# Kernel tuning notes

Hardware: AMD Instinct MI355X
Metric: run time of the kernel (lower is better)

## Reference

```python
import jax, jax.numpy as jnp
import numpy as np

B, T, J, D = 2048, 120, 24, 6
E = J * D            # embed_dim = 144
L = 4                # n_layer
NH = 8               # n_head
HD = E // NH         # head_dim = 18
H = 144              # d_model = gru hidden (must equal E, see forward concat)
FF = 4 * E           # transformer dim_feedforward
GIN = E + H          # gru input size


def _layernorm(x, w, b):
    m = x.mean(-1, keepdims=True)
    v = ((x - m) ** 2).mean(-1, keepdims=True)
    return (x - m) / jnp.sqrt(v + 1e-5) * w + b


def setup_inputs() -> dict:
    key = jax.random.key(0)
    ks = jax.random.split(key, 32)
    s = 0.02
    n = lambda k, sh: jax.random.normal(k, sh, jnp.float32) * s
    return {
        "seed": jax.random.normal(ks[0], (B, T, J, D), jnp.float32),
        "qkv_w": n(ks[1], (L, 3 * E, E)), "qkv_b": jnp.zeros((L, 3 * E), jnp.float32),
        "out_w": n(ks[2], (L, E, E)), "out_b": jnp.zeros((L, E), jnp.float32),
        "ln1_w": jnp.ones((L, E), jnp.float32), "ln1_b": jnp.zeros((L, E), jnp.float32),
        "ffn1_w": n(ks[3], (L, FF, E)), "ffn1_b": jnp.zeros((L, FF), jnp.float32),
        "ffn2_w": n(ks[4], (L, E, FF)), "ffn2_b": jnp.zeros((L, E), jnp.float32),
        "ln2_w": jnp.ones((L, E), jnp.float32), "ln2_b": jnp.zeros((L, E), jnp.float32),
        "proj_w": n(ks[5], (E, E)), "proj_b": jnp.zeros((E,), jnp.float32),
        "w_ih": n(ks[6], (3 * H, GIN)), "w_hh": n(ks[7], (3 * H, H)),
        "b_ih": jnp.zeros((3 * H,), jnp.float32), "b_hh": jnp.zeros((3 * H,), jnp.float32),
        "spl_w": n(ks[8], (E, H)), "spl_b": jnp.zeros((E,), jnp.float32),
        "future": 24,
    }


def reference(seed, qkv_w, qkv_b, out_w, out_b, ln1_w, ln1_b, ffn1_w, ffn1_b,
              ffn2_w, ffn2_b, ln2_w, ln2_b, proj_w, proj_b,
              w_ih, w_hh, b_ih, b_hh, spl_w, spl_b, future):
    Bv, Tv, Jv, Dv = seed.shape
    x = seed.reshape(Bv, Tv, Jv * Dv)  # [B, T, E]

    # --- TransformerEncoder (post-norm, relu, dropout=eval-mode identity) ---
    def layer_step(x, p):
        (qw, qb, ow, ob, l1w, l1b, f1w, f1b, f2w, f2b, l2w, l2b) = p
        qkv = jnp.einsum('bse,fe->bsf', x, qw) + qb          # [B,S,3E]
        q, k, v = jnp.split(qkv, 3, axis=-1)
        q = q.reshape(Bv, Tv, NH, HD)
        k = k.reshape(Bv, Tv, NH, HD)
        v = v.reshape(Bv, Tv, NH, HD)
        scores = jnp.einsum('bqhd,bkhd->bhqk', q, k) / jnp.sqrt(jnp.float32(HD))
        attn = jax.nn.softmax(scores, axis=-1)
        o = jnp.einsum('bhqk,bkhd->bqhd', attn, v).reshape(Bv, Tv, E)
        o = jnp.einsum('bse,fe->bsf', o, ow) + ob
        x = _layernorm(x + o, l1w, l1b)
        ff = jax.nn.relu(jnp.einsum('bse,fe->bsf', x, f1w) + f1b)
        ff = jnp.einsum('bsf,ef->bse', ff, f2w) + f2b
        x = _layernorm(x + ff, l2w, l2b)
        return x, None

    x, _ = jax.lax.scan(layer_step, x,
                        (qkv_w, qkv_b, out_w, out_b, ln1_w, ln1_b,
                         ffn1_w, ffn1_b, ffn2_w, ffn2_b, ln2_w, ln2_b))
    ctx = x.mean(axis=1) @ proj_w.T + proj_b               # [B, E]

    h0 = jnp.zeros((Bv, H), seed.dtype)
    inp0 = seed[:, -1].reshape(Bv, Jv * Dv)

    def step(carry, _):
        h, inp = carry
        xc = jnp.concatenate([inp, ctx], axis=-1)          # [B, E+H]
        gi = xc @ w_ih.T + b_ih                            # [B, 3H]
        gh = h @ w_hh.T + b_hh
        ir, iz, in_ = jnp.split(gi, 3, axis=-1)
        hr, hz, hn = jnp.split(gh, 3, axis=-1)
        r = jax.nn.sigmoid(ir + hr)
        z = jax.nn.sigmoid(iz + hz)
        n = jnp.tanh(in_ + r * hn)
        h_new = (1.0 - z) * n + z * h
        rot6d = h_new @ spl_w.T + spl_b                    # [B, E]
        return (h_new, rot6d), rot6d

    _, ys = jax.lax.scan(step, (h0, inp0), None, length=future)  # [future,B,E]
    return ys.transpose(1, 0, 2).reshape(Bv, future, Jv, Dv)
```

## Files before the change

### kernel.cpp

```cpp
#include <hip/hip_runtime.h>

#define B_   2048
#define T_   120
#define E_   144
#define L_   4
#define NH_  8
#define HD_  18
#define FF_  576
#define H_   144
#define GIN_ 288
#define TH_  432
#define FUT_ 24
#define BT_  (B_*T_)

typedef unsigned short u16;
typedef unsigned int   u32;

typedef __attribute__((ext_vector_type(8))) short short8v;
typedef __attribute__((ext_vector_type(4))) float f32x4;

__device__ __forceinline__ float bf2f(u16 u) {
    u32 x = ((u32)u) << 16;
    return __uint_as_float(x);
}
__device__ __forceinline__ u16 f2bf(float f) {
    u32 x = __float_as_uint(f);
    u32 r = (x + 0x7fffu + ((x >> 16) & 1u)) >> 16;
    return (u16)r;
}

struct F4 { float x, y, z, w; };

__device__ __forceinline__ F4 load4(const float* p) {
    float4 v = *(const float4*)p;
    return {v.x, v.y, v.z, v.w};
}
__device__ __forceinline__ void store1(float* p, float v) { *p = v; }
__device__ __forceinline__ void store1(u16* p, float v)   { *p = f2bf(v); }

__device__ __forceinline__ short8v wfrag(const u16* Wp, int tile, int NS, int s, int l) {
    return *(const short8v*)(Wp + (((size_t)tile * NS + s) * 64 + l) * 8);
}

__device__ __forceinline__ void gll16(const void* g, void* l) {
    __builtin_amdgcn_global_load_lds(
        (const __attribute__((address_space(1))) u32*)g,
        (__attribute__((address_space(3))) u32*)l, 16, 0, 0);
}

__device__ __forceinline__ void stage64(const u16* src, u32* lds, int tid) {
    const char* base = (const char*)src;
    char* lbase = (char*)lds;
    const int w = tid >> 6, l = tid & 63;
#pragma unroll
    for (int i = 0; i < 7; ++i) {
        int inst  = w * 7 + i;
        int chunk = inst * 64 + l;
        int row = chunk / 21;
        int col = chunk - row * 21;
        if (col > 17) col = 17;
        gll16(base + row * 288 + col * 16, lbase + inst * 1024);
    }
}

__global__ void wpack_kernel(const float* __restrict__ src, u16* __restrict__ dst,
                             int ntiles, int NS, int K, int sstr)
{
    int i = blockIdx.x * 256 + threadIdx.x;
    if (i >= ntiles * NS * 512) return;
    int e  = i & 7;
    int l  = (i >> 3) & 63;
    int c  = i >> 9;
    int s  = c % NS;
    int tile = c / NS;
    int li = l & 15, lg = l >> 4;
    int row = tile * 16 + li;
    int k   = s * 32 + lg * 8 + e;
    dst[i] = (k < K) ? f2bf(src[(size_t)row * sstr + k]) : (u16)0;
}

__global__ void cast_bf_kernel(const float* __restrict__ src, u16* __restrict__ dst,
                               int n2)
{
    int i = blockIdx.x * 256 + threadIdx.x;
    if (i >= n2) return;
    float2 t = ((const float2*)src)[i];
    ((u32*)dst)[i] = ((u32)f2bf(t.y) << 16) | (u32)f2bf(t.x);
}

template<typename OT>
__global__ __launch_bounds__(192) void gemm_mfma(
    const u16* __restrict__ A, const u16* __restrict__ Wb,
    const float* __restrict__ bias, OT* __restrict__ C, int M, int N)
{
    __shared__ u32 lds[64 * 84];

    const int tid = threadIdx.x;
    const int w   = tid >> 6;
    const int l   = tid & 63;
    const int lg  = l >> 4;
    const int li  = l & 15;
    const int bm  = blockIdx.y * 64;
    const int n0w = blockIdx.x * 144 + w * 48;
    const int t0  = blockIdx.x * 9 + w * 3;

    f32x4 acc[4][3];
#pragma unroll
    for (int rt = 0; rt < 4; rt++)
#pragma unroll
        for (int ct = 0; ct < 3; ct++) acc[rt][ct] = {0.f, 0.f, 0.f, 0.f};

    stage64(A + (size_t)bm * 144, lds, tid);
    __syncthreads();

    const u16* lds16 = (const u16*)lds;
#pragma unroll
    for (int s = 0; s < 5; ++s) {
        short8v bf[3];
#pragma unroll
        for (int ct = 0; ct < 3; ++ct)
            bf[ct] = wfrag(Wb, t0 + ct, 5, s, l);
        short8v af[4];
#pragma unroll
        for (int rt = 0; rt < 4; ++rt)
            af[rt] = *(const short8v*)(lds16 + (rt * 16 + li) * 168 + s * 32 + lg * 8);
#pragma unroll
        for (int rt = 0; rt < 4; ++rt)
#pragma unroll
            for (int ct = 0; ct < 3; ++ct)
                acc[rt][ct] = __builtin_amdgcn_mfma_f32_16x16x32_bf16(
                    af[rt], bf[ct], acc[rt][ct], 0, 0, 0);
    }

#pragma unroll
    for (int ct = 0; ct < 3; ++ct) {
        int col = n0w + ct * 16 + li;
        float bv = bias[col];
#pragma unroll
        for (int rt = 0; rt < 4; ++rt) {
#pragma unroll
            for (int j = 0; j < 4; ++j) {
                int row = bm + rt * 16 + lg * 4 + j;
                store1(&C[(size_t)row * N + col], acc[rt][ct][j] + bv);
            }
        }
    }
}

__global__ __launch_bounds__(192) void olnffn_kernel(
    const u16* __restrict__ ob, const u16* __restrict__ Wo,
    const float* __restrict__ ob_b, const float* __restrict__ res,
    const float* __restrict__ ln1w, const float* __restrict__ ln1b,
    const u16* __restrict__ W1, const float* __restrict__ b1,
    const u16* __restrict__ W2, const float* __restrict__ b2,
    const float* __restrict__ ln2w, const float* __restrict__ ln2b,
    u16* __restrict__ obf, float* __restrict__ of)
{
    __shared__ __align__(16) u16 Als[64 * 168];
    __shared__ u32 Fls[64 * 52];
    __shared__ float lnS[3][64], lnQ[3][64];

    const int tid = threadIdx.x;
    const int w   = tid >> 6;
    const int l   = tid & 63;
    const int lg  = l >> 4;
    const int li  = l & 15;
    const int bm  = blockIdx.x * 64;

    stage64(ob + (size_t)bm * 144, (u32*)Als, tid);
    __syncthreads();

    const u16* als = Als;
    u16* alsw = Als;
    u16* fls16 = (u16*)Fls;

    f32x4 acc[4][3];
#pragma unroll
    for (int rt = 0; rt < 4; rt++)
#pragma unroll
        for (int ct = 0; ct < 3; ct++) acc[rt][ct] = {0.f, 0.f, 0.f, 0.f};
#pragma unroll
    for (int s = 0; s < 5; ++s) {
        short8v bf[3];
#pragma unroll
        for (int ct = 0; ct < 3; ++ct)
            bf[ct] = wfrag(Wo, w * 3 + ct, 5, s, l);
        short8v af[4];
#pragma unroll
        for (int rt = 0; rt < 4; ++rt)
            af[rt] = *(const short8v*)(als + (rt * 16 + li) * 168 + s * 32 + lg * 8);
#pragma unroll
        for (int rt = 0; rt < 4; ++rt)
#pragma unroll
            for (int ct = 0; ct < 3; ++ct)
                acc[rt][ct] = __builtin_amdgcn_mfma_f32_16x16x32_bf16(
                    af[rt], bf[ct], acc[rt][ct], 0, 0, 0);
    }

    float vv[4][3][4];
#pragma unroll
    for (int ct = 0; ct < 3; ++ct) {
        int col = w * 48 + ct * 16 + li;
        float bv = ob_b[col];
#pragma unroll
        for (int rt = 0; rt < 4; ++rt)
#pragma unroll
            for (int j = 0; j < 4; ++j) {
                int row = bm + rt * 16 + lg * 4 + j;
                vv[rt][ct][j] = acc[rt][ct][j] + bv + res[(size_t)row * E_ + col];
            }
    }
#pragma unroll
    for (int rt = 0; rt < 4; ++rt)
#pragma unroll
        for (int j = 0; j < 4; ++j) {
            float s = vv[rt][0][j] + vv[rt][1][j] + vv[rt][2][j];
            float q = vv[rt][0][j] * vv[rt][0][j] + vv[rt][1][j] * vv[rt][1][j]
                    + vv[rt][2][j] * vv[rt][2][j];
#pragma unroll
            for (int off = 1; off < 16; off <<= 1) {
                s += __shfl_xor(s, off);
                q += __shfl_xor(q, off);
            }
            if (li == 0) {
                lnS[w][rt * 16 + lg * 4 + j] = s;
                lnQ[w][rt * 16 + lg * 4 + j] = q;
            }
        }
    __syncthreads();
#pragma unroll
    for (int rt = 0; rt < 4; ++rt)
#pragma unroll
        for (int j = 0; j < 4; ++j) {
            int r = rt * 16 + lg * 4 + j;
            float mean = (lnS[0][r] + lnS[1][r] + lnS[2][r]) * (1.f / 144.f);
            float var  = (lnQ[0][r] + lnQ[1][r] + lnQ[2][r]) * (1.f / 144.f) - mean * mean;
            float rstd = rsqrtf(var + 1e-5f);
#pragma unroll
            for (int ct = 0; ct < 3; ++ct) {
                int col = w * 48 + ct * 16 + li;
                float o = (vv[rt][ct][j] - mean) * rstd * ln1w[col] + ln1b[col];
                vv[rt][ct][j] = o;
                alsw[r * 168 + col] = f2bf(o);
            }
        }
    __syncthreads();

    f32x4 acc2[4][3];
#pragma unroll
    for (int rt = 0; rt < 4; rt++)
#pragma unroll
        for (int ct = 0; ct < 3; ct++) acc2[rt][ct] = {0.f, 0.f, 0.f, 0.f};

    for (int c = 0; c < 6; ++c) {
        f32x4 acc1[4][2];
#pragma unroll
        for (int rt = 0; rt < 4; rt++)
#pragma unroll
            for (int ct = 0; ct < 2; ct++) acc1[rt][ct] = {0.f, 0.f, 0.f, 0.f};
#pragma unroll
        for (int s = 0; s < 5; ++s) {
            short8v bf[2];
#pragma unroll
            for (int ct = 0; ct < 2; ++ct)
                bf[ct] = wfrag(W1, c * 6 + w * 2 + ct, 5, s, l);
            short8v af[4];
#pragma unroll
            for (int rt = 0; rt < 4; ++rt)
                af[rt] = *(const short8v*)(als + (rt * 16 + li) * 168 + s * 32 + lg * 8);
#pragma unroll
            for (int rt = 0; rt < 4; ++rt)
#pragma unroll
                for (int ct = 0; ct < 2; ++ct)
                    acc1[rt][ct] = __builtin_amdgcn_mfma_f32_16x16x32_bf16(
                        af[rt], bf[ct], acc1[rt][ct], 0, 0, 0);
        }
        __syncthreads();
#pragma unroll
        for (int ct = 0; ct < 2; ++ct) {
            int colc = w * 32 + ct * 16 + li;
            float bv = b1[c * 96 + colc];
#pragma unroll
            for (int rt = 0; rt < 4; ++rt)
#pragma unroll
                for (int j = 0; j < 4; ++j) {
                    int row = rt * 16 + lg * 4 + j;
                    float v = fmaxf(acc1[rt][ct][j] + bv, 0.f);
                    fls16[row * 104 + colc] = f2bf(v);
                }
        }
        __syncthreads();
#pragma unroll
        for (int s2 = 0; s2 < 3; ++s2) {
            short8v wf[3];
#pragma unroll
            for (int ct = 0; ct < 3; ++ct)
                wf[ct] = wfrag(W2, w * 3 + ct, 18, c * 3 + s2, l);
            short8v pf[4];
#pragma unroll
            for (int rt = 0; rt < 4; ++rt)
                pf[rt] = *(const short8v*)(fls16 + (rt * 16 + li) * 104 + s2 * 32 + lg * 8);
#pragma unroll
            for (int rt = 0; rt < 4; ++rt)
#pragma unroll
                for (int ct = 0; ct < 3; ++ct)
                    acc2[rt][ct] = __builtin_amdgcn_mfma_f32_16x16x32_bf16(
                        pf[rt], wf[ct], acc2[rt][ct], 0, 0, 0);
        }
    }

    float v2[4][3][4];
#pragma unroll
    for (int ct = 0; ct < 3; ++ct) {
        int col = w * 48 + ct * 16 + li;
        float bv = b2[col];
#pragma unroll
        for (int rt = 0; rt < 4; ++rt)
#pragma unroll
            for (int j = 0; j < 4; ++j)
                v2[rt][ct][j] = acc2[rt][ct][j] + bv + vv[rt][ct][j];
    }
#pragma unroll
    for (int rt = 0; rt < 4; ++rt)
#pragma unroll
        for (int j = 0; j < 4; ++j) {
            float s = v2[rt][0][j] + v2[rt][1][j] + v2[rt][2][j];
            float q = v2[rt][0][j] * v2[rt][0][j] + v2[rt][1][j] * v2[rt][1][j]
                    + v2[rt][2][j] * v2[rt][2][j];
#pragma unroll
            for (int off = 1; off < 16; off <<= 1) {
                s += __shfl_xor(s, off);
                q += __shfl_xor(q, off);
            }
            if (li == 0) {
                lnS[w][rt * 16 + lg * 4 + j] = s;
                lnQ[w][rt * 16 + lg * 4 + j] = q;
            }
        }
    __syncthreads();
#pragma unroll
    for (int rt = 0; rt < 4; ++rt)
#pragma unroll
        for (int j = 0; j < 4; ++j) {
            int r = rt * 16 + lg * 4 + j;
            float mean = (lnS[0][r] + lnS[1][r] + lnS[2][r]) * (1.f / 144.f);
            float var  = (lnQ[0][r] + lnQ[1][r] + lnQ[2][r]) * (1.f / 144.f) - mean * mean;
            float rstd = rsqrtf(var + 1e-5f);
            int row = bm + r;
#pragma unroll
            for (int ct = 0; ct < 3; ++ct) {
                int col = w * 48 + ct * 16 + li;
                float o = (v2[rt][ct][j] - mean) * rstd * ln2w[col] + ln2b[col];
                obf[(size_t)row * E_ + col] = f2bf(o);
                of[(size_t)row * E_ + col]  = o;
            }
        }
}

template<typename AT, typename OT, bool BIAS, bool RELU, bool RES>
__global__ __launch_bounds__(256) void gemm_kernel(
    const AT* __restrict__ A, const float* __restrict__ W, int ldw,
    const float* __restrict__ bias, const float* __restrict__ res,
    OT* __restrict__ C, int M, int N, int K)
{
    constexpr int BM = 64, BN = 64, BK = 16;
    __shared__ float As[BK][BM + 4];
    __shared__ float Ws[BK][BN + 4];
    const int tid = threadIdx.x;
    const int bm = blockIdx.y * BM;
    const int bn = blockIdx.x * BN;
    const int tx = tid & 15, ty = tid >> 4;
    const int lr = tid >> 2;
    const int lc = (tid & 3) << 2;

    float acc[4][4];
#pragma unroll
    for (int i = 0; i < 4; i++)
#pragma unroll
        for (int j = 0; j < 4; j++) acc[i][j] = 0.f;

    for (int k0 = 0; k0 < K; k0 += BK) {
        F4 av = load4(A + (size_t)(bm + lr) * K + k0 + lc);
        As[lc + 0][lr] = av.x; As[lc + 1][lr] = av.y;
        As[lc + 2][lr] = av.z; As[lc + 3][lr] = av.w;
        int n = bn + lr;
        F4 wv = {0.f, 0.f, 0.f, 0.f};
        if (n < N) {
            float4 t = *(const float4*)(W + (size_t)n * ldw + k0 + lc);
            wv = {t.x, t.y, t.z, t.w};
        }
        Ws[lc + 0][lr] = wv.x; Ws[lc + 1][lr] = wv.y;
        Ws[lc + 2][lr] = wv.z; Ws[lc + 3][lr] = wv.w;
        __syncthreads();
#pragma unroll
        for (int kk = 0; kk < BK; ++kk) {
            float a[4], wr[4];
#pragma unroll
            for (int i = 0; i < 4; i++) a[i] = As[kk][ty * 4 + i];
#pragma unroll
            for (int j = 0; j < 4; j++) wr[j] = Ws[kk][tx * 4 + j];
#pragma unroll
            for (int i = 0; i < 4; i++)
#pragma unroll
                for (int j = 0; j < 4; j++) acc[i][j] += a[i] * wr[j];
        }
        __syncthreads();
    }
#pragma unroll
    for (int i = 0; i < 4; i++) {
        int m = bm + ty * 4 + i;
#pragma unroll
        for (int j = 0; j < 4; j++) {
            int n = bn + tx * 4 + j;
            if (n < N) {
                float v = acc[i][j];
                if (BIAS) v += bias[n];
                if (RES)  v += res[(size_t)m * N + n];
                if (RELU) v = fmaxf(v, 0.f);
                store1(&C[(size_t)m * N + n], v);
            }
        }
    }
}

__global__ __launch_bounds__(256) void attn_kernel(const u16* __restrict__ qkv,
                                                   u16* __restrict__ o)
{
    constexpr int QS = 40;
    constexpr int VS = 136;
    __shared__ __align__(16) u16 Qs[128 * QS];
    __shared__ __align__(16) u16 Ks[128 * QS];
    __shared__ __align__(16) u16 Vt[32 * VS];
    __shared__ __align__(16) u16 Ps[4][16 * VS];

    const int bh = blockIdx.x;
    const int b = bh >> 3, h = bh & 7;
    const int tid = threadIdx.x;
    const int w = tid >> 6, l = tid & 63;
    const int lg = l >> 4, li = l & 15;

    {
        u32* z1 = (u32*)Qs;
        for (int i = tid; i < 128 * QS / 2; i += 256) z1[i] = 0;
        u32* z2 = (u32*)Ks;
        for (int i = tid; i < 128 * QS / 2; i += 256) z2[i] = 0;
        u32* z3 = (u32*)Vt;
        for (int i = tid; i < 32 * VS / 2; i += 256) z3[i] = 0;
    }
    __syncthreads();

    const u32* q32 = (const u32*)(qkv + (size_t)b * T_ * TH_);
    for (int idx = tid; idx < 120 * 9; idx += 256) {
        int t = idx / 9, dp = idx - t * 9;
        u32 qv = q32[t * 216 + 9 * h + dp];
        u32 kv = q32[t * 216 + 72 + 9 * h + dp];
        u32 vv = q32[t * 216 + 144 + 9 * h + dp];
        ((u32*)(Qs + t * QS))[dp] = qv;
        ((u32*)(Ks + t * QS))[dp] = kv;
        Vt[(2 * dp) * VS + t]     = (u16)(vv & 0xffffu);
        Vt[(2 * dp + 1) * VS + t] = (u16)(vv >> 16);
    }
    __syncthreads();

    const float scale = 0.23570226039551584f;
    u16* pw = &Ps[w][0];

    for (int mt = w * 2; mt < w * 2 + 2; ++mt) {
        short8v qf = *(const short8v*)(Qs + (mt * 16 + li) * QS + lg * 8);
        f32x4 sacc[8];
#pragma unroll
        for (int nt = 0; nt < 8; ++nt) sacc[nt] = {0.f, 0.f, 0.f, 0.f};
#pragma unroll
        for (int nt = 0; nt < 8; ++nt) {
            short8v kf = *(const short8v*)(Ks + (nt * 16 + li) * QS + lg * 8);
            sacc[nt] = __builtin_amdgcn_mfma_f32_16x16x32_bf16(qf, kf, sacc[nt], 0, 0, 0);
        }

        float invl[4];
#pragma unroll
        for (int j = 0; j < 4; ++j) {
            float v[8];
            float m = -1e30f;
#pragma unroll
            for (int nt = 0; nt < 8; ++nt) {
                float s = sacc[nt][j] * scale;
                if (nt == 7 && li >= 8) s = -1e30f;
                v[nt] = s;
                m = fmaxf(m, s);
            }
#pragma unroll
            for (int off = 1; off < 16; off <<= 1)
                m = fmaxf(m, __shfl_xor(m, off));
            float sum = 0.f;
#pragma unroll
            for (int nt = 0; nt < 8; ++nt) {
                float p = __expf(v[nt] - m);
                sum += p;
                pw[(lg * 4 + j) * VS + nt * 16 + li] = f2bf(p);
            }
#pragma unroll
            for (int off = 1; off < 16; off <<= 1)
                sum += __shfl_xor(sum, off);
            invl[j] = 1.f / sum;
        }

        f32x4 oacc[2] = {{0.f,0.f,0.f,0.f},{0.f,0.f,0.f,0.f}};
#pragma unroll
        for (int s = 0; s < 4; ++s) {
            short8v pf = *(const short8v*)(pw + li * VS + s * 32 + lg * 8);
#pragma unroll
            for (int dt = 0; dt < 2; ++dt) {
                short8v vf = *(const short8v*)(Vt + (dt * 16 + li) * VS + s * 32 + lg * 8);
                oacc[dt] = __builtin_amdgcn_mfma_f32_16x16x32_bf16(pf, vf, oacc[dt], 0, 0, 0);
            }
        }

        const int q0 = mt * 16 + lg * 4;
#pragma unroll
        for (int dt = 0; dt < 2; ++dt) {
            int d = dt * 16 + li;
            if (d < HD_) {
#pragma unroll
                for (int j = 0; j < 4; ++j) {
                    int q = q0 + j;
                    if (q < T_)
                        o[((size_t)b * T_ + q) * E_ + h * HD_ + d] =
                            f2bf(oacc[dt][j] * invl[j]);
                }
            }
        }
    }
}

__global__ void mean_kernel(const float* __restrict__ x, float* __restrict__ out,
                            int nb)
{
    int idx = blockIdx.x * blockDim.x + threadIdx.x;
    if (idx >= nb * E_) return;
    int b = idx / E_, e = idx % E_;
    const float* p = x + (size_t)b * T_ * E_ + e;
    float s = 0.f;
    for (int t = 0; t < T_; t++) s += p[(size_t)t * E_];
    out[idx] = s * (1.f / 120.f);
}

__device__ __forceinline__ float sigmoidf_(float x) {
    return 1.f / (1.f + __expf(-x));
}

#define GRU_M 16
__global__ __launch_bounds__(192) void gru_all_kernel(
    const float* __restrict__ seed,
    const float* __restrict__ gctx,
    const u16* __restrict__ WxB,
    const u16* __restrict__ WhB,
    const u16* __restrict__ SpB,
    const float* __restrict__ b_hh,
    const float* __restrict__ spl_b,
    float* __restrict__ out)
{
    __shared__ __align__(16) u16 xls[GRU_M * 168];
    __shared__ __align__(16) u16 hls[GRU_M * 168];

    const int tid = threadIdx.x;
    const int w = tid >> 6, l = tid & 63;
    const int lg = l >> 4, li = l & 15;
    const int b0 = blockIdx.x * GRU_M;
    const int fr = w * 48 + li;

    for (int i = tid; i < GRU_M * 84; i += 192) {
        ((u32*)xls)[i] = 0; ((u32*)hls)[i] = 0;
    }
    __syncthreads();
    for (int i = tid; i < GRU_M * 72; i += 192) {
        int r = i / 72, e2 = i - r * 72;
        float2 t = *(const float2*)(seed + (size_t)(b0 + r) * T_ * E_
                                    + (size_t)(T_ - 1) * E_ + 2 * e2);
        ((u32*)(xls + r * 168))[e2] = ((u32)f2bf(t.y) << 16) | (u32)f2bf(t.x);
    }

    float gctxv[3][3][4];
// ... 75 lines not shown
#pragma unroll
            for (int ct = 0; ct < 3; ++ct) {
                short8v bs = wfrag(SpB, w * 3 + ct, 5, s, l);
                aS[ct] = __builtin_amdgcn_mfma_f32_16x16x32_bf16(ah, bs, aS[ct], 0, 0, 0);
            }
        }
#pragma unroll
        for (int ct = 0; ct < 3; ++ct) {
            int col = fr + ct * 16;
#pragma unroll
            for (int j = 0; j < 4; ++j) {
                float rv = aS[ct][j] + splb[ct];
                out[(size_t)(b0 + lg * 4 + j) * (FUT_ * E_) + (size_t)st * E_ + col] = rv;
                xls[(lg * 4 + j) * 168 + col] = f2bf(rv);
            }
        }
        __syncthreads();
    }
}

extern "C" void kernel_launch(void* const* d_in, const int* in_sizes, int n_in,
                              void* d_out, int out_size, void* d_ws, size_t ws_size,
                              hipStream_t stream)
{
    const float* seed   = (const float*)d_in[0];
    const float* qkv_w  = (const float*)d_in[1];
    const float* qkv_b  = (const float*)d_in[2];
    const float* out_w  = (const float*)d_in[3];
    const float* out_b  = (const float*)d_in[4];
    const float* ln1_w  = (const float*)d_in[5];
    const float* ln1_b  = (const float*)d_in[6];
    const float* ffn1_w = (const float*)d_in[7];
    const float* ffn1_b = (const float*)d_in[8];
    const float* ffn2_w = (const float*)d_in[9];
    const float* ffn2_b = (const float*)d_in[10];
    const float* ln2_w  = (const float*)d_in[11];
    const float* ln2_b  = (const float*)d_in[12];
    const float* proj_w = (const float*)d_in[13];
    const float* proj_b = (const float*)d_in[14];
    const float* w_ih   = (const float*)d_in[15];
    const float* w_hh   = (const float*)d_in[16];
    const float* b_ih   = (const float*)d_in[17];
    const float* b_hh   = (const float*)d_in[18];
    const float* spl_w  = (const float*)d_in[19];
    const float* spl_b  = (const float*)d_in[20];

    const size_t qkvW_n  = (size_t)L_ * TH_ * 160;
    const size_t outW_n  = (size_t)L_ * E_ * 160;
    const size_t ffn1W_n = (size_t)L_ * FF_ * 160;
    const size_t ffn2W_n = (size_t)L_ * E_ * 576;
    const size_t wxW_n   = (size_t)TH_ * 160;
    const size_t whW_n   = (size_t)TH_ * 160;
    const size_t spW_n   = (size_t)E_ * 160;
    const size_t wbytes  = (qkvW_n + outW_n + ffn1W_n + ffn2W_n
                            + wxW_n + whW_n + spW_n) * 2;

    const size_t persist = (size_t)B_ * 4 * (E_ + E_ + TH_) + wbytes;

    int nc = 16;
    for (int c = 1; c <= 16; c <<= 1) {
        size_t rows = (size_t)(B_ / c) * T_;
        size_t need = persist + rows * 2016;
        if (need <= ws_size) { nc = c; break; }
    }
    const int BC = B_ / nc;
    const int CR = BC * T_;

    char* wsp = (char*)d_ws;
    u16*   xbf   = (u16*)wsp;   wsp += (size_t)CR * E_ * 2;
    float* xres  = (float*)wsp; wsp += (size_t)CR * E_ * 4;
    u16*   qf    = (u16*)wsp;   wsp += (size_t)CR * TH_ * 2;
    u16*   ob    = (u16*)wsp;   wsp += (size_t)CR * E_ * 2;
    float* ctxm  = (float*)wsp; wsp += (size_t)B_ * E_ * 4;
    float* ctx   = (float*)wsp; wsp += (size_t)B_ * E_ * 4;
    float* gctx  = (float*)wsp; wsp += (size_t)B_ * TH_ * 4;
    u16* qkvWb   = (u16*)wsp;   wsp += qkvW_n * 2;
    u16* outWb   = (u16*)wsp;   wsp += outW_n * 2;
    u16* ffn1Wb  = (u16*)wsp;   wsp += ffn1W_n * 2;
    u16* ffn2Wb  = (u16*)wsp;   wsp += ffn2W_n * 2;
    u16* wxB     = (u16*)wsp;   wsp += wxW_n * 2;
    u16* whB     = (u16*)wsp;   wsp += whW_n * 2;
    u16* splWb   = (u16*)wsp;   wsp += spW_n * 2;

    wpack_kernel<<<(int)((qkvW_n + 255) / 256), 256, 0, stream>>>(qkv_w, qkvWb, L_ * 27, 5, 144, 144);
    wpack_kernel<<<(int)((outW_n + 255) / 256), 256, 0, stream>>>(out_w, outWb, L_ * 9, 5, 144, 144);
    wpack_kernel<<<(int)((ffn1W_n + 255) / 256), 256, 0, stream>>>(ffn1_w, ffn1Wb, L_ * 36, 5, 144, 144);
    wpack_kernel<<<(int)((ffn2W_n + 255) / 256), 256, 0, stream>>>(ffn2_w, ffn2Wb, L_ * 9, 18, 576, 576);
    wpack_kernel<<<(int)((wxW_n + 255) / 256), 256, 0, stream>>>(w_ih, wxB, 27, 5, 144, GIN_);
    wpack_kernel<<<(int)((whW_n + 255) / 256), 256, 0, stream>>>(w_hh, whB, 27, 5, 144, 144);
    wpack_kernel<<<(int)((spW_n + 255) / 256), 256, 0, stream>>>(spl_w, splWb, 9, 5, 144, 144);

    auto grid = [](int M, int N) { return dim3((N + 63) / 64, M / 64); };

    for (int c = 0; c < nc; c++) {
        const int b0 = c * BC;
        cast_bf_kernel<<<(CR * 72 + 255) / 256, 256, 0, stream>>>(
            seed + (size_t)b0 * T_ * E_, xbf, CR * 72);
        const float* resIn = seed + (size_t)b0 * T_ * E_;
        for (int l = 0; l < L_; l++) {
            gemm_mfma<u16><<<dim3(3, CR / 64), 192, 0, stream>>>(
                xbf, qkvWb + (size_t)l * TH_ * 160, qkv_b + (size_t)l * TH_,
                qf, CR, TH_);
            attn_kernel<<<BC * NH_, 256, 0, stream>>>(qf, ob);
            olnffn_kernel<<<CR / 64, 192, 0, stream>>>(
                ob, outWb + (size_t)l * E_ * 160, out_b + (size_t)l * E_, resIn,
                ln1_w + (size_t)l * E_, ln1_b + (size_t)l * E_,
                ffn1Wb + (size_t)l * FF_ * 160, ffn1_b + (size_t)l * FF_,
                ffn2Wb + (size_t)l * E_ * 576, ffn2_b + (size_t)l * E_,
                ln2_w + (size_t)l * E_, ln2_b + (size_t)l * E_, xbf, xres);
            resIn = xres;
        }
        mean_kernel<<<(BC * E_ + 255) / 256, 256, 0, stream>>>(xres, ctxm + (size_t)b0 * E_, BC);
    }

    gemm_kernel<float, float, true, false, false><<<grid(B_, E_), 256, 0, stream>>>(
        ctxm, proj_w, E_, proj_b, nullptr, ctx, B_, E_, E_);
    gemm_kernel<float, float, true, false, false><<<grid(B_, TH_), 256, 0, stream>>>(
        ctx, w_ih + E_, GIN_, b_ih, nullptr, gctx, B_, TH_, E_);

    gru_all_kernel<<<B_ / GRU_M, 192, 0, stream>>>(
        seed, gctx, wxB, whB, splWb, b_hh, spl_b, (float*)d_out);
}
```

Before: 2.863 ms.

## Fuse QKV, attention, out-proj, LN and FFN into one per-sequence layer kernel

Replaces the per-layer QKV GEMM, attention and out-proj/LN/FFN kernels with a single layer_kernel that processes one batch sequence (120 rows) per block. QKV results and attention outputs stay in LDS instead of round-tripping through global memory, and the batch-chunk loop is removed so all sequences run in one launch per layer. The residual is now read from the bf16 activations (except in layer 0), which lowers precision. The large LDS footprint and launch bounds of one block per CU may limit occupancy and latency hiding.

```diff
diff --git a/kernel.cpp b/kernel.cpp
--- a/kernel.cpp
+++ b/kernel.cpp
@@ -30,7 +30,6 @@
 }
 
 struct F4 { float x, y, z, w; };
-
 __device__ __forceinline__ F4 load4(const float* p) {
     float4 v = *(const float4*)p;
     return {v.x, v.y, v.z, v.w};
@@ -48,19 +47,14 @@
         (__attribute__((address_space(3))) u32*)l, 16, 0, 0);
 }
 
-__device__ __forceinline__ void stage64(const u16* src, u32* lds, int tid) {
-    const char* base = (const char*)src;
-    char* lbase = (char*)lds;
-    const int w = tid >> 6, l = tid & 63;
-#pragma unroll
-    for (int i = 0; i < 7; ++i) {
-        int inst  = w * 7 + i;
-        int chunk = inst * 64 + l;
-        int row = chunk / 21;
-        int col = chunk - row * 21;
-        if (col > 17) col = 17;
-        gll16(base + row * 288 + col * 16, lbase + inst * 1024);
-    }
+__device__ __forceinline__ short8v qk_frag(const u16* rowp, int colbase, int lg) {
+    u32 u0 = 0, u1 = 0, u2 = 0, u3 = 0;
+    const u32* p = (const u32*)(rowp + colbase + lg * 8);
+    if (lg < 2) { u0 = p[0]; u1 = p[1]; u2 = p[2]; u3 = p[3]; }
+    else if (lg == 2) { u0 = p[0]; }
+    union { u32 u[4]; short8v v; } r;
+    r.u[0] = u0; r.u[1] = u1; r.u[2] = u2; r.u[3] = u3;
+    return r.v;
 }
 
 __global__ void wpack_kernel(const float* __restrict__ src, u16* __restrict__ dst,
@@ -88,271 +82,360 @@
     ((u32*)dst)[i] = ((u32)f2bf(t.y) << 16) | (u32)f2bf(t.x);
 }
 
-template<typename OT>
-__global__ __launch_bounds__(192) void gemm_mfma(
-    const u16* __restrict__ A, const u16* __restrict__ Wb,
-    const float* __restrict__ bias, OT* __restrict__ C, int M, int N)
-{
-    __shared__ u32 lds[64 * 84];
-
-    const int tid = threadIdx.x;
-    const int w   = tid >> 6;
-    const int l   = tid & 63;
-    const int lg  = l >> 4;
-    const int li  = l & 15;
-    const int bm  = blockIdx.y * 64;
-    const int n0w = blockIdx.x * 144 + w * 48;
-    const int t0  = blockIdx.x * 9 + w * 3;
-
-    f32x4 acc[4][3];
-#pragma unroll
-    for (int rt = 0; rt < 4; rt++)
-#pragma unroll
-        for (int ct = 0; ct < 3; ct++) acc[rt][ct] = {0.f, 0.f, 0.f, 0.f};
-
-    stage64(A + (size_t)bm * 144, lds, tid);
-    __syncthreads();
-
-    const u16* lds16 = (const u16*)lds;
-#pragma unroll
-    for (int s = 0; s < 5; ++s) {
-        short8v bf[3];
-#pragma unroll
-        for (int ct = 0; ct < 3; ++ct)
-            bf[ct] = wfrag(Wb, t0 + ct, 5, s, l);
-        short8v af[4];
-#pragma unroll
-        for (int rt = 0; rt < 4; ++rt)
-            af[rt] = *(const short8v*)(lds16 + (rt * 16 + li) * 168 + s * 32 + lg * 8);
-#pragma unroll
-        for (int rt = 0; rt < 4; ++rt)
-#pragma unroll
-            for (int ct = 0; ct < 3; ++ct)
-                acc[rt][ct] = __builtin_amdgcn_mfma_f32_16x16x32_bf16(
-                    af[rt], bf[ct], acc[rt][ct], 0, 0, 0);
-    }
-
-#pragma unroll
-    for (int ct = 0; ct < 3; ++ct) {
-        int col = n0w + ct * 16 + li;
-        float bv = bias[col];
-#pragma unroll
-        for (int rt = 0; rt < 4; ++rt) {
-#pragma unroll
-            for (int j = 0; j < 4; ++j) {
-                int row = bm + rt * 16 + lg * 4 + j;
-                store1(&C[(size_t)row * N + col], acc[rt][ct][j] + bv);
-            }
-        }
-    }
-}
-
-__global__ __launch_bounds__(192) void olnffn_kernel(
-    const u16* __restrict__ ob, const u16* __restrict__ Wo,
-    const float* __restrict__ ob_b, const float* __restrict__ res,
+template<bool RESF32, bool WF32>
+__global__ __launch_bounds__(256, 1) void layer_kernel(
+    const u16* __restrict__ xin,
+    const float* __restrict__ resf, const u16* __restrict__ resb,
+    const u16* __restrict__ Wqkv, const float* __restrict__ bqkv,
+    const u16* __restrict__ Wo, const float* __restrict__ bo,
     const float* __restrict__ ln1w, const float* __restrict__ ln1b,
     const u16* __restrict__ W1, const float* __restrict__ b1,
     const u16* __restrict__ W2, const float* __restrict__ b2,
     const float* __restrict__ ln2w, const float* __restrict__ ln2b,
     u16* __restrict__ obf, float* __restrict__ of)
 {
-    __shared__ __align__(16) u16 Als[64 * 168];
-    __shared__ u32 Fls[64 * 52];
-    __shared__ float lnS[3][64], lnQ[3][64];
+    __shared__ __align__(16) u16 Xls[21504];
+    __shared__ __align__(16) u16 QKV[128 * 440];
 
     const int tid = threadIdx.x;
-    const int w   = tid >> 6;
-    const int l   = tid & 63;
-    const int lg  = l >> 4;
-    const int li  = l & 15;
-    const int bm  = blockIdx.x * 64;
-
-    stage64(ob + (size_t)bm * 144, (u32*)Als, tid);
-    __syncthreads();
-
-    const u16* als = Als;
-    u16* alsw = Als;
-    u16* fls16 = (u16*)Fls;
-
-    f32x4 acc[4][3];
-#pragma unroll
-    for (int rt = 0; rt < 4; rt++)
-#pragma unroll
-        for (int ct = 0; ct < 3; ct++) acc[rt][ct] = {0.f, 0.f, 0.f, 0.f};
+    const int w  = tid >> 6, l = tid & 63;
+    const int lg = l >> 4,  li = l & 15;
+    const size_t grow0 = (size_t)blockIdx.x * T_;
+
+    for (int i = tid; i < 672; i += 256) ((u32*)Xls)[10080 + i] = 0;
+    {
+        const char* src = (const char*)(xin + grow0 * E_);
+        char* dst = (char*)Xls;
+#pragma unroll
+        for (int i = 0; i < 10; ++i) {
+            int inst = w * 10 + i;
+            int chunk = inst * 64 + l;
+            if (chunk < 2520) {
+                int row = chunk / 21, col = chunk - row * 21;
+                if (col > 17) col = 17;
+                gll16(src + row * 288 + col * 16, dst + inst * 1024);
+            }
+        }
+    }
+    __syncthreads();
+
+#pragma unroll
+    for (int ci = 0; ci < 7; ++ci) {
+        int ct = w + 4 * ci;
+        if (ct < 27) {
+            f32x4 acc[8];
+#pragma unroll
+            for (int rt = 0; rt < 8; ++rt) acc[rt] = {0.f, 0.f, 0.f, 0.f};
+#pragma unroll
+            for (int s = 0; s < 5; ++s) {
+                short8v bf = wfrag(Wqkv, ct, 5, s, l);
+#pragma unroll
+                for (int rt = 0; rt < 8; ++rt) {
+                    short8v af = *(const short8v*)(Xls + (rt * 16 + li) * 168 + s * 32 + lg * 8);
+                    acc[rt] = __builtin_amdgcn_mfma_f32_16x16x32_bf16(af, bf, acc[rt], 0, 0, 0);
+                }
+            }
+            int col = ct * 16 + li;
+            float bv = bqkv[col];
+#pragma unroll
+            for (int rt = 0; rt < 8; ++rt)
+#pragma unroll
+                for (int j = 0; j < 4; ++j)
+                    QKV[(rt * 16 + lg * 4 + j) * 440 + col] = f2bf(acc[rt][j] + bv);
+        }
+    }
+    __syncthreads();
+
+    {
+        const float scale = 0.23570226039551584f;
+        u16* Pw = Xls + w * 2176;
+        for (int h = 0; h < NH_; ++h) {
+            const int qc = h * HD_;
+            short8v kf[8];
+#pragma unroll
+            for (int nt = 0; nt < 8; ++nt)
+                kf[nt] = qk_frag(QKV + (nt * 16 + li) * 440, E_ + qc, lg);
+            short8v vf[2][4];
+#pragma unroll
+            for (int dt = 0; dt < 2; ++dt) {
+                int d = dt * 16 + li;
+#pragma unroll
+                for (int s = 0; s < 4; ++s) {
+                    union { u16 h16[8]; short8v v; } r;
+#pragma unroll
+                    for (int e = 0; e < 8; ++e)
+                        r.h16[e] = (d < HD_)
+                            ? QKV[(s * 32 + lg * 8 + e) * 440 + 2 * E_ + qc + d]
+                            : (u16)0;
+                    vf[dt][s] = r.v;
+                }
+            }
+#pragma unroll
+            for (int qi = 0; qi < 2; ++qi) {
+                int qt = 2 * w + qi;
+                short8v qf = qk_frag(QKV + (qt * 16 + li) * 440, qc, lg);
+                f32x4 sacc[8];
+#pragma unroll
+                for (int nt = 0; nt < 8; ++nt) sacc[nt] = {0.f, 0.f, 0.f, 0.f};
+#pragma unroll
+                for (int nt = 0; nt < 8; ++nt)
+                    sacc[nt] = __builtin_amdgcn_mfma_f32_16x16x32_bf16(qf, kf[nt], sacc[nt], 0, 0, 0);
+
+                float invl[4];
+#pragma unroll
+                for (int j = 0; j < 4; ++j) {
+                    float v[8];
+                    float m = -1e30f;
+#pragma unroll
+                    for (int nt = 0; nt < 8; ++nt) {
+                        float s = sacc[nt][j] * scale;
+                        if (nt == 7 && li >= 8) s = -1e30f;
+                        v[nt] = s;
+                        m = fmaxf(m, s);
+                    }
+#pragma unroll
+                    for (int off = 1; off < 16; off <<= 1)
+                        m = fmaxf(m, __shfl_xor(m, off));
+                    float sum = 0.f;
+#pragma unroll
+                    for (int nt = 0; nt < 8; ++nt) {
+                        float p = __expf(v[nt] - m);
+                        sum += p;
+                        Pw[(lg * 4 + j) * 136 + nt * 16 + li] = f2bf(p);
+                    }
+#pragma unroll
+                    for (int off = 1; off < 16; off <<= 1)
+                        sum += __shfl_xor(sum, off);
+                    invl[j] = 1.f / sum;
+                }
+
+                f32x4 oacc[2] = {{0.f,0.f,0.f,0.f},{0.f,0.f,0.f,0.f}};
+#pragma unroll
+                for (int s = 0; s < 4; ++s) {
+                    short8v pf = *(const short8v*)(Pw + li * 136 + s * 32 + lg * 8);
+#pragma unroll
+                    for (int dt = 0; dt < 2; ++dt)
+                        oacc[dt] = __builtin_amdgcn_mfma_f32_16x16x32_bf16(pf, vf[dt][s], oacc[dt], 0, 0, 0);
+                }
+#pragma unroll
+                for (int dt = 0; dt < 2; ++dt) {
+                    int d = dt * 16 + li;
+                    if (d < HD_) {
+#pragma unroll
+                        for (int j = 0; j < 4; ++j)
+                            QKV[(qt * 16 + lg * 4 + j) * 440 + qc + d] =
+                                f2bf(oacc[dt][j] * invl[j]);
+                    }
+                }
+            }
+        }
+    }
+    __syncthreads();
+
+    float* lnS = (float*)(Xls + 10240);
+    float* lnQ = (float*)(Xls + 11264);
+
+    float rr[3][8][4];
+#pragma unroll
+    for (int ci = 0; ci < 3; ++ci) {
+        int tile = w + 4 * ci;
+        if (tile < 9) {
+            int col = tile * 16 + li;
+#pragma unroll
+            for (int rt = 0; rt < 8; ++rt)
+#pragma unroll
+                for (int j = 0; j < 4; ++j) {
+                    int r = rt * 16 + lg * 4 + j;
+                    if (r > 119) r = 119;
+                    rr[ci][rt][j] = RESF32 ? resf[(grow0 + r) * E_ + col]
+                                           : bf2f(resb[(grow0 + r) * E_ + col]);
+                }
+        }
+    }
+
+    f32x4 acc[3][8];
+#pragma unroll
+    for (int ci = 0; ci < 3; ++ci)
+#pragma unroll
+        for (int rt = 0; rt < 8; ++rt) acc[ci][rt] = {0.f, 0.f, 0.f, 0.f};
 #pragma unroll
     for (int s = 0; s < 5; ++s) {
-        short8v bf[3];
-#pragma unroll
-        for (int ct = 0; ct < 3; ++ct)
-            bf[ct] = wfrag(Wo, w * 3 + ct, 5, s, l);
-        short8v af[4];
-#pragma unroll
-        for (int rt = 0; rt < 4; ++rt)
-            af[rt] = *(const short8v*)(als + (rt * 16 + li) * 168 + s * 32 + lg * 8);
-#pragma unroll
-        for (int rt = 0; rt < 4; ++rt)
-#pragma unroll
-            for (int ct = 0; ct < 3; ++ct)
-                acc[rt][ct] = __builtin_amdgcn_mfma_f32_16x16x32_bf16(
-                    af[rt], bf[ct], acc[rt][ct], 0, 0, 0);
-    }
-
-    float vv[4][3][4];
-#pragma unroll
-    for (int ct = 0; ct < 3; ++ct) {
-        int col = w * 48 + ct * 16 + li;
-        float bv = ob_b[col];
-#pragma unroll
-        for (int rt = 0; rt < 4; ++rt)
-#pragma unroll
-            for (int j = 0; j < 4; ++j) {
-                int row = bm + rt * 16 + lg * 4 + j;
-                vv[rt][ct][j] = acc[rt][ct][j] + bv + res[(size_t)row * E_ + col];
-            }
-    }
-#pragma unroll
-    for (int rt = 0; rt < 4; ++rt)
+        short8v bfv[3];
+#pragma unroll
+        for (int ci = 0; ci < 3; ++ci) {
+            int tile = w + 4 * ci;
+            if (tile < 9) bfv[ci] = wfrag(Wo, tile, 5, s, l);
+        }
+#pragma unroll
+        for (int rt = 0; rt < 8; ++rt) {
+            short8v af = *(const short8v*)(QKV + (rt * 16 + li) * 440 + s * 32 + lg * 8);
+#pragma unroll
+            for (int ci = 0; ci < 3; ++ci)
+                if (w + 4 * ci < 9)
+                    acc[ci][rt] = __builtin_amdgcn_mfma_f32_16x16x32_bf16(af, bfv[ci], acc[ci][rt], 0, 0, 0);
+        }
+    }
+
+    float vv[3][8][4];
+#pragma unroll
+    for (int ci = 0; ci < 3; ++ci) {
+        int tile = w + 4 * ci;
+        if (tile < 9) {
+            float bv = bo[tile * 16 + li];
+#pragma unroll
+            for (int rt = 0; rt < 8; ++rt)
+#pragma unroll
+                for (int j = 0; j < 4; ++j)
+                    vv[ci][rt][j] = acc[ci][rt][j] + bv + rr[ci][rt][j];
+        }
+    }
+#pragma unroll
+    for (int rt = 0; rt < 8; ++rt)
 #pragma unroll
         for (int j = 0; j < 4; ++j) {
-            float s = vv[rt][0][j] + vv[rt][1][j] + vv[rt][2][j];
-            float q = vv[rt][0][j] * vv[rt][0][j] + vv[rt][1][j] * vv[rt][1][j]
-                    + vv[rt][2][j] * vv[rt][2][j];
+            float s = 0.f, q = 0.f;
+#pragma unroll
+            for (int ci = 0; ci < 3; ++ci)
+                if (w + 4 * ci < 9) { s += vv[ci][rt][j]; q += vv[ci][rt][j] * vv[ci][rt][j]; }
 #pragma unroll
             for (int off = 1; off < 16; off <<= 1) {
                 s += __shfl_xor(s, off);
                 q += __shfl_xor(q, off);
             }
             if (li == 0) {
-                lnS[w][rt * 16 + lg * 4 + j] = s;
-                lnQ[w][rt * 16 + lg * 4 + j] = q;
-            }
-        }
-    __syncthreads();
-#pragma unroll
-    for (int rt = 0; rt < 4; ++rt)
+                lnS[w * 128 + rt * 16 + lg * 4 + j] = s;
+                lnQ[w * 128 + rt * 16 + lg * 4 + j] = q;
+            }
+        }
+    __syncthreads();
+#pragma unroll
+    for (int rt = 0; rt < 8; ++rt)
 #pragma unroll
         for (int j = 0; j < 4; ++j) {
             int r = rt * 16 + lg * 4 + j;
-            float mean = (lnS[0][r] + lnS[1][r] + lnS[2][r]) * (1.f / 144.f);
-            float var  = (lnQ[0][r] + lnQ[1][r] + lnQ[2][r]) * (1.f / 144.f) - mean * mean;
+            float s = lnS[r] + lnS[128 + r] + lnS[256 + r] + lnS[384 + r];
+            float q = lnQ[r] + lnQ[128 + r] + lnQ[256 + r] + lnQ[384 + r];
+            float mean = s * (1.f / 144.f);
+            float var  = q * (1.f / 144.f) - mean * mean;
             float rstd = rsqrtf(var + 1e-5f);
 #pragma unroll
-            for (int ct = 0; ct < 3; ++ct) {
-                int col = w * 48 + ct * 16 + li;
-                float o = (vv[rt][ct][j] - mean) * rstd * ln1w[col] + ln1b[col];
-                vv[rt][ct][j] = o;
-                alsw[r * 168 + col] = f2bf(o);
-            }
-        }
-    __syncthreads();
-
-    f32x4 acc2[4][3];
-#pragma unroll
-    for (int rt = 0; rt < 4; rt++)
-#pragma unroll
-        for (int ct = 0; ct < 3; ct++) acc2[rt][ct] = {0.f, 0.f, 0.f, 0.f};
-
-    for (int c = 0; c < 6; ++c) {
-        f32x4 acc1[4][2];
-#pragma unroll
-        for (int rt = 0; rt < 4; rt++)
-#pragma unroll
-            for (int ct = 0; ct < 2; ct++) acc1[rt][ct] = {0.f, 0.f, 0.f, 0.f};
+            for (int ci = 0; ci < 3; ++ci) {
+                int tile = w + 4 * ci;
+                if (tile < 9) {
+                    int col = tile * 16 + li;
+                    float o = (vv[ci][rt][j] - mean) * rstd * ln1w[col] + ln1b[col];
+                    vv[ci][rt][j] = o;
+                    QKV[r * 440 + col] = f2bf(o);
+                }
+            }
+        }
+    __syncthreads();
+
+    u16* Fls = Xls;
+    f32x4 acc2[3][8];
+#pragma unroll
+    for (int ci = 0; ci < 3; ++ci)
+#pragma unroll
+        for (int rt = 0; rt < 8; ++rt) acc2[ci][rt] = {0.f, 0.f, 0.f, 0.f};
+
+    for (int c = 0; c < 9; ++c) {
+        f32x4 acc1[8];
+#pragma unroll
+        for (int rt = 0; rt < 8; ++rt) acc1[rt] = {0.f, 0.f, 0.f, 0.f};
 #pragma unroll
         for (int s = 0; s < 5; ++s) {
-            short8v bf[2];
-#pragma unroll
-            for (int ct = 0; ct < 2; ++ct)
-                bf[ct] = wfrag(W1, c * 6 + w * 2 + ct, 5, s, l);
-            short8v af[4];
-#pragma unroll
-            for (int rt = 0; rt < 4; ++rt)
-                af[rt] = *(const short8v*)(als + (rt * 16 + li) * 168 + s * 32 + lg * 8);
-#pragma unroll
-            for (int rt = 0; rt < 4; ++rt)
-#pragma unroll
-                for (int ct = 0; ct < 2; ++ct)
-                    acc1[rt][ct] = __builtin_amdgcn_mfma_f32_16x16x32_bf16(
-                        af[rt], bf[ct], acc1[rt][ct], 0, 0, 0);
+            short8v bf = wfrag(W1, c * 4 + w, 5, s, l);
+#pragma unroll
+            for (int rt = 0; rt < 8; ++rt) {
+                short8v af = *(const short8v*)(QKV + (rt * 16 + li) * 440 + s * 32 + lg * 8);
+                acc1[rt] = __builtin_amdgcn_mfma_f32_16x16x32_bf16(af, bf, acc1[rt], 0, 0, 0);
+            }
         }
         __syncthreads();
-#pragma unroll
-        for (int ct = 0; ct < 2; ++ct) {
-            int colc = w * 32 + ct * 16 + li;
-            float bv = b1[c * 96 + colc];
-#pragma unroll
-            for (int rt = 0; rt < 4; ++rt)
+        {
+            int colc = w * 16 + li;
+            float bv = b1[c * 64 + colc];
+#pragma unroll
+            for (int rt = 0; rt < 8; ++rt)
 #pragma unroll
                 for (int j = 0; j < 4; ++j) {
-                    int row = rt * 16 + lg * 4 + j;
-                    float v = fmaxf(acc1[rt][ct][j] + bv, 0.f);
-                    fls16[row * 104 + colc] = f2bf(v);
+                    float v = fmaxf(acc1[rt][j] + bv, 0.f);
+                    Fls[(rt * 16 + lg * 4 + j) * 72 + colc] = f2bf(v);
                 }
         }
         __syncthreads();
 #pragma unroll
-        for (int s2 = 0; s2 < 3; ++s2) {
-            short8v wf[3];
-#pragma unroll
-            for (int ct = 0; ct < 3; ++ct)
-                wf[ct] = wfrag(W2, w * 3 + ct, 18, c * 3 + s2, l);
-            short8v pf[4];
-#pragma unroll
-            for (int rt = 0; rt < 4; ++rt)
-                pf[rt] = *(const short8v*)(fls16 + (rt * 16 + li) * 104 + s2 * 32 + lg * 8);
-#pragma unroll
-            for (int rt = 0; rt < 4; ++rt)
-#pragma unroll
-                for (int ct = 0; ct < 3; ++ct)
-                    acc2[rt][ct] = __builtin_amdgcn_mfma_f32_16x16x32_bf16(
-                        pf[rt], wf[ct], acc2[rt][ct], 0, 0, 0);
-        }
-    }
-
-    float v2[4][3][4];
-#pragma unroll
-    for (int ct = 0; ct < 3; ++ct) {
-        int col = w * 48 + ct * 16 + li;
-        float bv = b2[col];
-#pragma unroll
-        for (int rt = 0; rt < 4; ++rt)
-#pragma unroll
-            for (int j = 0; j < 4; ++j)
-                v2[rt][ct][j] = acc2[rt][ct][j] + bv + vv[rt][ct][j];
-    }
-#pragma unroll
-    for (int rt = 0; rt < 4; ++rt)
+        for (int s2 = 0; s2 < 2; ++s2) {
+            short8v bfw[3];
+#pragma unroll
+            for (int ci = 0; ci < 3; ++ci) {
+                int tile = w + 4 * ci;
+                if (tile < 9) bfw[ci] = wfrag(W2, tile, 18, c * 2 + s2, l);
+            }
+#pragma unroll
+            for (int rt = 0; rt < 8; ++rt) {
+                short8v pf = *(const short8v*)(Fls + (rt * 16 + li) * 72 + s2 * 32 + lg * 8);
+#pragma unroll
+                for (int ci = 0; ci < 3; ++ci)
+                    if (w + 4 * ci < 9)
+                        acc2[ci][rt] = __builtin_amdgcn_mfma_f32_16x16x32_bf16(pf, bfw[ci], acc2[ci][rt], 0, 0, 0);
+            }
+        }
+    }
+
+#pragma unroll
+    for (int ci = 0; ci < 3; ++ci) {
+        int tile = w + 4 * ci;
+        if (tile < 9) {
+            float bv = b2[tile * 16 + li];
+#pragma unroll
+            for (int rt = 0; rt < 8; ++rt)
+#pragma unroll
+                for (int j = 0; j < 4; ++j)
+                    vv[ci][rt][j] = acc2[ci][rt][j] + bv + vv[ci][rt][j];
+        }
+    }
+    __syncthreads();
+#pragma unroll
+    for (int rt = 0; rt < 8; ++rt)
 #pragma unroll
         for (int j = 0; j < 4; ++j) {
-            float s = v2[rt][0][j] + v2[rt][1][j] + v2[rt][2][j];
-            float q = v2[rt][0][j] * v2[rt][0][j] + v2[rt][1][j] * v2[rt][1][j]
-                    + v2[rt][2][j] * v2[rt][2][j];
+            float s = 0.f, q = 0.f;
+#pragma unroll
+            for (int ci = 0; ci < 3; ++ci)
+                if (w + 4 * ci < 9) { s += vv[ci][rt][j]; q += vv[ci][rt][j] * vv[ci][rt][j]; }
 #pragma unroll
             for (int off = 1; off < 16; off <<= 1) {
                 s += __shfl_xor(s, off);
                 q += __shfl_xor(q, off);
             }
             if (li == 0) {
-                lnS[w][rt * 16 + lg * 4 + j] = s;
-                lnQ[w][rt * 16 + lg * 4 + j] = q;
-            }
-        }
-    __syncthreads();
-#pragma unroll
-    for (int rt = 0; rt < 4; ++rt)
+                lnS[w * 128 + rt * 16 + lg * 4 + j] = s;
+                lnQ[w * 128 + rt * 16 + lg * 4 + j] = q;
+            }
+        }
+    __syncthreads();
+#pragma unroll
+    for (int rt = 0; rt < 8; ++rt)
 #pragma unroll
         for (int j = 0; j < 4; ++j) {
             int r = rt * 16 + lg * 4 + j;
-            float mean = (lnS[0][r] + lnS[1][r] + lnS[2][r]) * (1.f / 144.f);
-            float var  = (lnQ[0][r] + lnQ[1][r] + lnQ[2][r]) * (1.f / 144.f) - mean * mean;
-            float rstd = rsqrtf(var + 1e-5f);
-            int row = bm + r;
-#pragma unroll
-            for (int ct = 0; ct < 3; ++ct) {
-                int col = w * 48 + ct * 16 + li;
-                float o = (v2[rt][ct][j] - mean) * rstd * ln2w[col] + ln2b[col];
-                obf[(size_t)row * E_ + col] = f2bf(o);
-                of[(size_t)row * E_ + col]  = o;
+            if (r < T_) {
+                float s = lnS[r] + lnS[128 + r] + lnS[256 + r] + lnS[384 + r];
+                float q = lnQ[r] + lnQ[128 + r] + lnQ[256 + r] + lnQ[384 + r];
+                float mean = s * (1.f / 144.f);
+                float var  = q * (1.f / 144.f) - mean * mean;
+                float rstd = rsqrtf(var + 1e-5f);
+#pragma unroll
+                for (int ci = 0; ci < 3; ++ci) {
+                    int tile = w + 4 * ci;
+                    if (tile < 9) {
+                        int col = tile * 16 + li;
+                        float o = (vv[ci][rt][j] - mean) * rstd * ln2w[col] + ln2b[col];
+                        obf[(grow0 + r) * E_ + col] = f2bf(o);
+                        if (WF32) of[(grow0 + r) * E_ + col] = o;
+                    }
+                }
             }
         }
 }
@@ -418,115 +501,6 @@
                 if (RES)  v += res[(size_t)m * N + n];
                 if (RELU) v = fmaxf(v, 0.f);
                 store1(&C[(size_t)m * N + n], v);
-            }
-        }
-    }
-}
-
-__global__ __launch_bounds__(256) void attn_kernel(const u16* __restrict__ qkv,
-                                                   u16* __restrict__ o)
-{
-    constexpr int QS = 40;
-    constexpr int VS = 136;
-    __shared__ __align__(16) u16 Qs[128 * QS];
-    __shared__ __align__(16) u16 Ks[128 * QS];
-    __shared__ __align__(16) u16 Vt[32 * VS];
-    __shared__ __align__(16) u16 Ps[4][16 * VS];
-
-    const int bh = blockIdx.x;
-    const int b = bh >> 3, h = bh & 7;
-    const int tid = threadIdx.x;
-    const int w = tid >> 6, l = tid & 63;
-    const int lg = l >> 4, li = l & 15;
-
-    {
-        u32* z1 = (u32*)Qs;
-        for (int i = tid; i < 128 * QS / 2; i += 256) z1[i] = 0;
-        u32* z2 = (u32*)Ks;
-        for (int i = tid; i < 128 * QS / 2; i += 256) z2[i] = 0;
-        u32* z3 = (u32*)Vt;
-        for (int i = tid; i < 32 * VS / 2; i += 256) z3[i] = 0;
-    }
-    __syncthreads();
-
-    const u32* q32 = (const u32*)(qkv + (size_t)b * T_ * TH_);
-    for (int idx = tid; idx < 120 * 9; idx += 256) {
-        int t = idx / 9, dp = idx - t * 9;
-        u32 qv = q32[t * 216 + 9 * h + dp];
-        u32 kv = q32[t * 216 + 72 + 9 * h + dp];
-        u32 vv = q32[t * 216 + 144 + 9 * h + dp];
-        ((u32*)(Qs + t * QS))[dp] = qv;
-        ((u32*)(Ks + t * QS))[dp] = kv;
-        Vt[(2 * dp) * VS + t]     = (u16)(vv & 0xffffu);
-        Vt[(2 * dp + 1) * VS + t] = (u16)(vv >> 16);
-    }
-    __syncthreads();
-
-    const float scale = 0.23570226039551584f;
-    u16* pw = &Ps[w][0];
-
-    for (int mt = w * 2; mt < w * 2 + 2; ++mt) {
-        short8v qf = *(const short8v*)(Qs + (mt * 16 + li) * QS + lg * 8);
-        f32x4 sacc[8];
-#pragma unroll
-        for (int nt = 0; nt < 8; ++nt) sacc[nt] = {0.f, 0.f, 0.f, 0.f};
-#pragma unroll
-        for (int nt = 0; nt < 8; ++nt) {
-            short8v kf = *(const short8v*)(Ks + (nt * 16 + li) * QS + lg * 8);
-            sacc[nt] = __builtin_amdgcn_mfma_f32_16x16x32_bf16(qf, kf, sacc[nt], 0, 0, 0);
-        }
-
-        float invl[4];
-#pragma unroll
-        for (int j = 0; j < 4; ++j) {
-            float v[8];
-            float m = -1e30f;
-#pragma unroll
-            for (int nt = 0; nt < 8; ++nt) {
-                float s = sacc[nt][j] * scale;
-                if (nt == 7 && li >= 8) s = -1e30f;
-                v[nt] = s;
-                m = fmaxf(m, s);
-            }
-#pragma unroll
-            for (int off = 1; off < 16; off <<= 1)
-                m = fmaxf(m, __shfl_xor(m, off));
-            float sum = 0.f;
-#pragma unroll
-            for (int nt = 0; nt < 8; ++nt) {
-                float p = __expf(v[nt] - m);
-                sum += p;
-                pw[(lg * 4 + j) * VS + nt * 16 + li] = f2bf(p);
-            }
-#pragma unroll
-            for (int off = 1; off < 16; off <<= 1)
-                sum += __shfl_xor(sum, off);
-            invl[j] = 1.f / sum;
-        }
-
-        f32x4 oacc[2] = {{0.f,0.f,0.f,0.f},{0.f,0.f,0.f,0.f}};
-#pragma unroll
-        for (int s = 0; s < 4; ++s) {
-            short8v pf = *(const short8v*)(pw + li * VS + s * 32 + lg * 8);
-#pragma unroll
-            for (int dt = 0; dt < 2; ++dt) {
-                short8v vf = *(const short8v*)(Vt + (dt * 16 + li) * VS + s * 32 + lg * 8);
-                oacc[dt] = __builtin_amdgcn_mfma_f32_16x16x32_bf16(pf, vf, oacc[dt], 0, 0, 0);
-            }
-        }
-
-        const int q0 = mt * 16 + lg * 4;
-#pragma unroll
-        for (int dt = 0; dt < 2; ++dt) {
-            int d = dt * 16 + li;
-            if (d < HD_) {
-#pragma unroll
-                for (int j = 0; j < 4; ++j) {
-                    int q = q0 + j;
-                    if (q < T_)
-                        o[((size_t)b * T_ + q) * E_ + h * HD_ + d] =
-                            f2bf(oacc[dt][j] * invl[j]);
-                }
             }
         }
     }
@@ -708,25 +682,10 @@
     const size_t wxW_n   = (size_t)TH_ * 160;
     const size_t whW_n   = (size_t)TH_ * 160;
     const size_t spW_n   = (size_t)E_ * 160;
-    const size_t wbytes  = (qkvW_n + outW_n + ffn1W_n + ffn2W_n
-                            + wxW_n + whW_n + spW_n) * 2;
-
-    const size_t persist = (size_t)B_ * 4 * (E_ + E_ + TH_) + wbytes;
-
-    int nc = 16;
-    for (int c = 1; c <= 16; c <<= 1) {
-        size_t rows = (size_t)(B_ / c) * T_;
-        size_t need = persist + rows * 2016;
-        if (need <= ws_size) { nc = c; break; }
-    }
-    const int BC = B_ / nc;
-    const int CR = BC * T_;
 
     char* wsp = (char*)d_ws;
-    u16*   xbf   = (u16*)wsp;   wsp += (size_t)CR * E_ * 2;
-    float* xres  = (float*)wsp; wsp += (size_t)CR * E_ * 4;
-    u16*   qf    = (u16*)wsp;   wsp += (size_t)CR * TH_ * 2;
-    u16*   ob    = (u16*)wsp;   wsp += (size_t)CR * E_ * 2;
+    u16*   xbf   = (u16*)wsp;   wsp += (size_t)BT_ * E_ * 2;
+    float* xres  = (float*)wsp; wsp += (size_t)BT_ * E_ * 4;
     float* ctxm  = (float*)wsp; wsp += (size_t)B_ * E_ * 4;
     float* ctx   = (float*)wsp; wsp += (size_t)B_ * E_ * 4;
     float* gctx  = (float*)wsp; wsp += (size_t)B_ * TH_ * 4;
@@ -746,29 +705,39 @@
     wpack_kernel<<<(int)((whW_n + 255) / 256), 256, 0, stream>>>(w_hh, whB, 27, 5, 144, 144);
     wpack_kernel<<<(int)((spW_n + 255) / 256), 256, 0, stream>>>(spl_w, splWb, 9, 5, 144, 144);
 
+    cast_bf_kernel<<<(BT_ * 72 + 255) / 256, 256, 0, stream>>>(seed, xbf, BT_ * 72);
+
+    for (int l = 0; l < L_; l++) {
+        const u16* Wq = qkvWb + (size_t)l * TH_ * 160;
+        const u16* Wo = outWb + (size_t)l * E_ * 160;
+        const u16* W1 = ffn1Wb + (size_t)l * FF_ * 160;
+        const u16* W2 = ffn2Wb + (size_t)l * E_ * 576;
+        if (l == 0) {
+            layer_kernel<true, false><<<B_, 256, 0, stream>>>(
+                xbf, seed, nullptr, Wq, qkv_b + (size_t)l * TH_,
+                Wo, out_b + (size_t)l * E_,
+                ln1_w + (size_t)l * E_, ln1_b + (size_t)l * E_,
+                W1, ffn1_b + (size_t)l * FF_, W2, ffn2_b + (size_t)l * E_,
+                ln2_w + (size_t)l * E_, ln2_b + (size_t)l * E_, xbf, nullptr);
+        } else if (l < 3) {
+            layer_kernel<false, false><<<B_, 256, 0, stream>>>(
+                xbf, nullptr, xbf, Wq, qkv_b + (size_t)l * TH_,
+                Wo, out_b + (size_t)l * E_,
+                ln1_w + (size_t)l * E_, ln1_b + (size_t)l * E_,
+                W1, ffn1_b + (size_t)l * FF_, W2, ffn2_b + (size_t)l * E_,
+                ln2_w + (size_t)l * E_, ln2_b + (size_t)l * E_, xbf, nullptr);
+        } else {
+            layer_kernel<false, true><<<B_, 256, 0, stream>>>(
+                xbf, nullptr, xbf, Wq, qkv_b + (size_t)l * TH_,
+                Wo, out_b + (size_t)l * E_,
+                ln1_w + (size_t)l * E_, ln1_b + (size_t)l * E_,
+                W1, ffn1_b + (size_t)l * FF_, W2, ffn2_b + (size_t)l * E_,
+                ln2_w + (size_t)l * E_, ln2_b + (size_t)l * E_, xbf, xres);
+        }
+    }
+
     auto grid = [](int M, int N) { return dim3((N + 63) / 64, M / 64); };
-
-    for (int c = 0; c < nc; c++) {
-        const int b0 = c * BC;
-        cast_bf_kernel<<<(CR * 72 + 255) / 256, 256, 0, stream>>>(
-            seed + (size_t)b0 * T_ * E_, xbf, CR * 72);
-        const float* resIn = seed + (size_t)b0 * T_ * E_;
-        for (int l = 0; l < L_; l++) {
-            gemm_mfma<u16><<<dim3(3, CR / 64), 192, 0, stream>>>(
-                xbf, qkvWb + (size_t)l * TH_ * 160, qkv_b + (size_t)l * TH_,
-                qf, CR, TH_);
-            attn_kernel<<<BC * NH_, 256, 0, stream>>>(qf, ob);
-            olnffn_kernel<<<CR / 64, 192, 0, stream>>>(
-                ob, outWb + (size_t)l * E_ * 160, out_b + (size_t)l * E_, resIn,
-                ln1_w + (size_t)l * E_, ln1_b + (size_t)l * E_,
-                ffn1Wb + (size_t)l * FF_ * 160, ffn1_b + (size_t)l * FF_,
-                ffn2Wb + (size_t)l * E_ * 576, ffn2_b + (size_t)l * E_,
-                ln2_w + (size_t)l * E_, ln2_b + (size_t)l * E_, xbf, xres);
-            resIn = xres;
-        }
-        mean_kernel<<<(BC * E_ + 255) / 256, 256, 0, stream>>>(xres, ctxm + (size_t)b0 * E_, BC);
-    }
-
+    mean_kernel<<<(B_ * E_ + 255) / 256, 256, 0, stream>>>(xres, ctxm, B_);
     gemm_kernel<float, float, true, false, false><<<grid(B_, E_), 256, 0, stream>>>(
         ctxm, proj_w, E_, proj_b, nullptr, ctx, B_, E_, E_);
     gemm_kernel<float, float, true, false, false><<<grid(B_, TH_), 256, 0, stream>>>(
```

New measurement: 4.213 ms. +47.2%, slower.
